# Performance work log

Hardware: AMD Instinct MI355X
Metric: run time of the kernel (lower is better)

## Reference

```python
import jax, jax.numpy as jnp
import numpy as np

DIM = 1024
H = 16
D = DIM // H  # head_dim = 64
SCALE = D ** (-0.5)


def _gate_mlp(x, w1, b1, w2, b2):
    # Linear -> ReLU -> Linear -> Sigmoid
    h = jax.nn.relu(x @ w1 + b1)
    return jax.nn.sigmoid(h @ w2 + b2)


def _heads(t, B, N):
    # [B,N,C] -> [B,H,N,D]
    return t.reshape(B, N, H, D).transpose(0, 2, 1, 3)


def setup_inputs() -> dict:
    key = jax.random.key(0)
    ks = jax.random.split(key, 12)
    s = 1.0 / np.sqrt(DIM)
    inp = {
        "x1": jax.random.normal(ks[0], (4, 4096, DIM), jnp.float32),
        "x2": jax.random.normal(ks[1], (4, 4096, DIM), jnp.float32),
        # kv projections (no bias, qkv_bias=False); stored as [in, out]
        "Wkv1": jax.random.normal(ks[2], (DIM, 2 * DIM), jnp.float32) * s,
        "Wkv2": jax.random.normal(ks[3], (DIM, 2 * DIM), jnp.float32) * s,
        # gate MLP 1
        "g1_w1": jax.random.normal(ks[4], (DIM, DIM), jnp.float32) * s,
        "g1_b1": jnp.zeros((DIM,), jnp.float32),
        "g1_w2": jax.random.normal(ks[5], (DIM, DIM), jnp.float32) * s,
        "g1_b2": jnp.zeros((DIM,), jnp.float32),
        # gate MLP 2
        "g2_w1": jax.random.normal(ks[6], (DIM, DIM), jnp.float32) * s,
        "g2_b1": jnp.zeros((DIM,), jnp.float32),
        "g2_w2": jax.random.normal(ks[7], (DIM, DIM), jnp.float32) * s,
        "g2_b2": jnp.zeros((DIM,), jnp.float32),
    }
    return inp


def reference(x1, x2, Wkv1, Wkv2, g1_w1, g1_b1, g1_w2, g1_b2, g2_w1, g2_b1, g2_w2, g2_b2):
    B, N, C = x1.shape

    q1 = _heads(x1, B, N)  # [B,H,N,D]
    q2 = _heads(x2, B, N)

    kv1 = (x1 @ Wkv1).reshape(B, N, 2, H, D).transpose(2, 0, 3, 1, 4)
    k1, v1 = kv1[0], kv1[1]  # [B,H,N,D]
    kv2 = (x2 @ Wkv2).reshape(B, N, 2, H, D).transpose(2, 0, 3, 1, 4)
    k2, v2 = kv2[0], kv2[1]

    gate1 = _heads(_gate_mlp(x1, g1_w1, g1_b1, g1_w2, g1_b2), B, N)
    gate2 = _heads(_gate_mlp(x2, g2_w1, g2_b1, g2_w2, g2_b2), B, N)

    # context: k^T @ (v*gate) -> [B,H,D,D], softmax over first D axis (dim=-2)
    ctx1 = jnp.einsum('bhnd,bhne->bhde', k1, v1 * gate1) * SCALE
    ctx1 = jax.nn.softmax(ctx1, axis=-2)
    ctx2 = jnp.einsum('bhnd,bhne->bhde', k2, v2 * gate2) * SCALE
    ctx2 = jax.nn.softmax(ctx2, axis=-2)

    # cross: x1 attends via ctx2, x2 via ctx1
    o1 = jnp.einsum('bhnd,bhde->bhne', q1, ctx2).transpose(0, 2, 1, 3).reshape(B, N, C)
    o2 = jnp.einsum('bhnd,bhde->bhne', q2, ctx1).transpose(0, 2, 1, 3).reshape(B, N, C)
    return (o1, o2)
```

## Files before the change

### kernel.cpp

```cpp
#include <hip/hip_runtime.h>
#include <hip/hip_bf16.h>

typedef __attribute__((ext_vector_type(8))) short bf16x8_t;
typedef __attribute__((ext_vector_type(4))) float f32x4_t;
typedef unsigned short u16;
typedef unsigned int u32;

#define GLL16(gp, lp) \
    __builtin_amdgcn_global_load_lds((const __attribute__((address_space(1))) u32*)(gp), \
                                     (__attribute__((address_space(3))) u32*)(lp), 16, 0, 0)

__device__ __forceinline__ float bf2f(unsigned int u16v) {
    union { unsigned int i; float f; } c;
    c.i = (u16v & 0xffffu) << 16;
    return c.f;
}
__device__ __forceinline__ unsigned short f2bf(float f) {
    union { float f; unsigned int i; } c; c.f = f;
    unsigned int x = c.i;
    unsigned int r = (x + 0x7fffu + ((x >> 16) & 1u)) >> 16;
    return (unsigned short)r;
}


__global__ void cast_x2_kernel(const float* __restrict__ x1, const float* __restrict__ x2,
                               u16* __restrict__ h1, u16* __restrict__ h2, int n4) {
    int i = blockIdx.x * blockDim.x + threadIdx.x;
    int stride = gridDim.x * blockDim.x;
    for (; i < n4; i += stride) {
        float4 v = *(const float4*)(x1 + (size_t)i * 4);
        ushort4 h;
        h.x = f2bf(v.x); h.y = f2bf(v.y); h.z = f2bf(v.z); h.w = f2bf(v.w);
        *(ushort4*)(h1 + (size_t)i * 4) = h;
        v = *(const float4*)(x2 + (size_t)i * 4);
        h.x = f2bf(v.x); h.y = f2bf(v.y); h.z = f2bf(v.z); h.w = f2bf(v.w);
        *(ushort4*)(h2 + (size_t)i * 4) = h;
    }
}

__global__ __launch_bounds__(256) void cast_wt4_kernel(
    const float* __restrict__ W0, const float* __restrict__ W1,
    const float* __restrict__ W2, const float* __restrict__ W3,
    u16* __restrict__ T0, u16* __restrict__ T1,
    u16* __restrict__ T2, u16* __restrict__ T3,
    int K, int N) {
    const float* W = (blockIdx.z == 0) ? W0 : (blockIdx.z == 1) ? W1 : (blockIdx.z == 2) ? W2 : W3;
    u16* Wt = (blockIdx.z == 0) ? T0 : (blockIdx.z == 1) ? T1 : (blockIdx.z == 2) ? T2 : T3;
    __shared__ u16 tile[32][33];
    int c0 = blockIdx.x * 32, k0 = blockIdx.y * 32;
    int tx = threadIdx.x & 31, ty = threadIdx.x >> 5;
#pragma unroll
    for (int i = 0; i < 4; ++i) {
        int k = k0 + ty + i * 8;
        tile[ty + i * 8][tx] = f2bf(W[(size_t)k * N + c0 + tx]);
    }
    __syncthreads();
#pragma unroll
    for (int i = 0; i < 4; ++i) {
        int c = c0 + ty + i * 8;
        Wt[(size_t)c * K + k0 + tx] = tile[tx][ty + i * 8];
    }
}

__global__ __launch_bounds__(256) void cast_wt_split2_kernel(
    const float* __restrict__ W0, const float* __restrict__ W1,
    u16* __restrict__ H0, u16* __restrict__ L0,
    u16* __restrict__ H1, u16* __restrict__ L1,
    int K, int N) {
    const float* W = blockIdx.z ? W1 : W0;
    u16* Wh = blockIdx.z ? H1 : H0;
    u16* Wl = blockIdx.z ? L1 : L0;
    __shared__ u16 th[32][33];
    __shared__ u16 tl[32][33];
    int c0 = blockIdx.x * 32, k0 = blockIdx.y * 32;
    int tx = threadIdx.x & 31, ty = threadIdx.x >> 5;
#pragma unroll
    for (int i = 0; i < 4; ++i) {
        int k = k0 + ty + i * 8;
        float f = W[(size_t)k * N + c0 + tx];
        unsigned short h = f2bf(f);
        th[ty + i * 8][tx] = h;
        tl[ty + i * 8][tx] = f2bf(f - bf2f(h));
    }
    __syncthreads();
#pragma unroll
    for (int i = 0; i < 4; ++i) {
        int c = c0 + ty + i * 8;
        Wh[(size_t)c * K + k0 + tx] = th[tx][ty + i * 8];
        Wl[(size_t)c * K + k0 + tx] = tl[tx][ty + i * 8];
    }
}


__device__ __forceinline__ void stage32(u16* lds_buf, const u16* __restrict__ gbase, int tid) {
#pragma unroll
    for (int g = 0; g < 2; ++g) {
        int c = tid + g * 256;
        int row = c >> 2, qp = c & 3;
        int qs = qp ^ ((row >> 1) & 3);
        GLL16(gbase + (size_t)row * 1024 + qs * 8, lds_buf + c * 8);
    }
}

template <int EPI>
__global__ __launch_bounds__(256, 4) void gemm128_kernel(
    const u16* __restrict__ Ah,
    const u16* __restrict__ Bh, const u16* __restrict__ Bl,
    const float* __restrict__ bias,
    u16* __restrict__ out_bf, float* __restrict__ out_f,
    float* __restrict__ gate_vg, float* __restrict__ kout,
    int N)
{
    __shared__ u16 As[2][4096];
    __shared__ u16 Bs[2][4096];
    const int NT = (EPI == 2) ? 64 : 32;

    int nwg = 128 * (N >> 7);
    int wg = blockIdx.y * 128 + blockIdx.x;
    int cpx = nwg >> 3;
    wg = (wg & 7) * cpx + (wg >> 3);
    int bx = wg & 127, by = wg >> 7;
    int row0 = bx << 7, col0 = by << 7;

    const int tid = threadIdx.x;
    const int lane = tid & 63;
    const int w = tid >> 6;
    const int wm = w >> 1, wn = w & 1;
    const int fr = lane & 15, fq = lane >> 4;

    const u16* Ab0 = Ah + (size_t)row0 * 1024;
    auto aslice = [&](int s) { return Ab0 + s * 32; };
    auto bbase = [&](int kt) -> const u16* {
        if (EPI == 2) return ((kt & 1) ? Bl : Bh) + (size_t)col0 * 1024 + (kt >> 1) * 32;
        return Bh + (size_t)col0 * 1024 + kt * 32;
    };

    f32x4_t acc[4][4];
#pragma unroll
    for (int m = 0; m < 4; ++m)
#pragma unroll
        for (int n = 0; n < 4; ++n) acc[m][n] = (f32x4_t)(0.0f);

    const int slot = (fq ^ ((fr >> 1) & 3)) * 8;
    int aoff[4], boff[4];
#pragma unroll
    for (int m = 0; m < 4; ++m) aoff[m] = (wm * 64 + m * 16 + fr) * 32 + slot;
#pragma unroll
    for (int n = 0; n < 4; ++n) boff[n] = (wn * 64 + n * 16 + fr) * 32 + slot;

    stage32(As[0], aslice(0), tid);
    stage32(Bs[0], bbase(0), tid);

    for (int kt = 0; kt < NT; ++kt) {
        __syncthreads();

        if (kt + 1 < NT) {
            stage32(Bs[(kt + 1) & 1], bbase(kt + 1), tid);
            if (EPI == 2) {
                int s1 = (kt >> 1) + 1;
                if ((kt & 1) == 0 && s1 < 32)
                    stage32(As[s1 & 1], aslice(s1), tid);
            } else {
                stage32(As[(kt + 1) & 1], aslice(kt + 1), tid);
            }
        }

        const int ab = (EPI == 2) ? ((kt >> 1) & 1) : (kt & 1);
        const int bb = kt & 1;
        bf16x8_t a[4], b[4];
#pragma unroll
        for (int m = 0; m < 4; ++m) a[m] = *(const bf16x8_t*)&As[ab][aoff[m]];
#pragma unroll
        for (int n = 0; n < 4; ++n) b[n] = *(const bf16x8_t*)&Bs[bb][boff[n]];
#pragma unroll
        for (int m = 0; m < 4; ++m)
#pragma unroll
            for (int n = 0; n < 4; ++n)
                acc[m][n] = __builtin_amdgcn_mfma_f32_16x16x32_bf16(a[m], b[n], acc[m][n], 0, 0, 0);
    }

#pragma unroll
    for (int m = 0; m < 4; ++m) {
        int row = row0 + wm * 64 + m * 16 + fq * 4;
#pragma unroll
        for (int n = 0; n < 4; ++n) {
            int col = col0 + wn * 64 + n * 16 + fr;
            if (EPI == 0) {
                float bv = bias[col];
#pragma unroll
                for (int rr = 0; rr < 4; ++rr)
                    out_bf[(size_t)(row + rr) * N + col] = f2bf(fmaxf(acc[m][n][rr] + bv, 0.0f));
            } else if (EPI == 1) {
                float bv = bias[col];
#pragma unroll
                for (int rr = 0; rr < 4; ++rr)
                    out_f[(size_t)(row + rr) * N + col] = 1.0f / (1.0f + __expf(-(acc[m][n][rr] + bv)));
            } else {
                if (col < 1024) {
#pragma unroll
                    for (int rr = 0; rr < 4; ++rr)
                        kout[(size_t)(row + rr) * 1024 + col] = acc[m][n][rr];
                } else {
#pragma unroll
                    for (int rr = 0; rr < 4; ++rr) {
                        size_t idx = (size_t)(row + rr) * 1024 + (col - 1024);
                        gate_vg[idx] = acc[m][n][rr] * gate_vg[idx];
                    }
                }
            }
        }
    }
}

__global__ __launch_bounds__(256) void ctx_part_kernel(
    const float* __restrict__ kmat,
    const float* __restrict__ vmat,
    float* __restrict__ part)
{
    int bh = blockIdx.x & 63;
    int p  = blockIdx.x >> 6;
    int b = bh >> 4, h = bh & 15;
    int n0 = p * 512;
    __shared__ float ks[128][64];
    __shared__ float vs[128][64];
    int t = threadIdx.x;
    int dg = t & 15, eg = t >> 4;
    float acc[4][4];
#pragma unroll
    for (int i = 0; i < 4; ++i)
#pragma unroll
        for (int j = 0; j < 4; ++j) acc[i][j] = 0.0f;

    const float* kb = kmat + (size_t)b * 4096 * 1024 + h * 64;
    const float* vb = vmat + (size_t)b * 4096 * 1024 + h * 64;

    for (int c0 = 0; c0 < 512; c0 += 128) {
        __syncthreads();
#pragma unroll
        for (int s = 0; s < 8; ++s) {
            int ci = t + s * 256;
            int r = ci >> 4, o4 = (ci & 15) * 4;
            size_t g = (size_t)(n0 + c0 + r) * 1024 + o4;
            *(float4*)(&ks[r][o4]) = *(const float4*)(kb + g);
            *(float4*)(&vs[r][o4]) = *(const float4*)(vb + g);
        }
        __syncthreads();
#pragma unroll 4
        for (int n = 0; n < 128; ++n) {
            float4 k4 = *(const float4*)(&ks[n][dg * 4]);
            float4 v4 = *(const float4*)(&vs[n][eg * 4]);
            acc[0][0] += k4.x * v4.x; acc[0][1] += k4.x * v4.y; acc[0][2] += k4.x * v4.z; acc[0][3] += k4.x * v4.w;
            acc[1][0] += k4.y * v4.x; acc[1][1] += k4.y * v4.y; acc[1][2] += k4.y * v4.z; acc[1][3] += k4.y * v4.w;
            acc[2][0] += k4.z * v4.x; acc[2][1] += k4.z * v4.y; acc[2][2] += k4.z * v4.z; acc[2][3] += k4.z * v4.w;
            acc[3][0] += k4.w * v4.x; acc[3][1] += k4.w * v4.y; acc[3][2] += k4.w * v4.z; acc[3][3] += k4.w * v4.w;
        }
    }
    float* pp = part + ((size_t)(p * 64 + bh)) * 64 * 64;
#pragma unroll
    for (int i = 0; i < 4; ++i)
#pragma unroll
        for (int j = 0; j < 4; ++j)
            pp[(dg * 4 + i) * 64 + (eg * 4 + j)] = acc[i][j];
}

__global__ __launch_bounds__(256) void softmax_ctx_kernel(const float* __restrict__ part,
                                                          float* __restrict__ ctx) {
    int bh = blockIdx.x;
    int t = threadIdx.x;
    int e = t & 63, dq = t >> 6;
    __shared__ float red[4][68];
    float loc[16];
    float m = -1e30f;
#pragma unroll
    for (int i = 0; i < 16; ++i) {
        int d = dq * 16 + i;
        float s = 0.f;
#pragma unroll
        for (int p = 0; p < 8; ++p)
            s += part[(((size_t)(p * 64 + bh)) * 64 + d) * 64 + e];
        s *= 0.125f;
        loc[i] = s;
        m = fmaxf(m, s);
    }
    red[dq][e] = m;
    __syncthreads();
    float M = fmaxf(fmaxf(red[0][e], red[1][e]), fmaxf(red[2][e], red[3][e]));
    float sum = 0.f;
#pragma unroll
    for (int i = 0; i < 16; ++i) {
        float v = __expf(loc[i] - M);
        loc[i] = v;
        sum += v;
    }
    __syncthreads();
    red[dq][e] = sum;
    __syncthreads();
    float inv = 1.0f / (red[0][e] + red[1][e] + red[2][e] + red[3][e]);
#pragma unroll
    for (int i = 0; i < 16; ++i) {
        int d = dq * 16 + i;
        ctx[((size_t)bh * 64 + d) * 64 + e] = loc[i] * inv;
    }
}

__global__ __launch_bounds__(256) void out_gemm_kernel(
    const float* __restrict__ x1, const float* __restrict__ x2,
    const float* __restrict__ ctxA,
    const float* __restrict__ ctxB,
    float* __restrict__ out)
{
    int id = blockIdx.x;
    int s = id >> 12;
    int r = id & 4095;
    int nc = r & 63;
    int h = (r >> 6) & 15;
    int b = r >> 10;
    const float* x = s ? x2 : x1;
    const float* ctx = s ? ctxB : ctxA;
    float* o = out + (size_t)s * 16777216;
    size_t r0 = (size_t)b * 4096 + nc * 64;
    __shared__ float xs[64][65];
    __shared__ float cs[64][64];
    int t = threadIdx.x;
    for (int idx = t; idx < 4096; idx += 256) {
        int rr = idx >> 6, d = idx & 63;
        xs[rr][d] = x[(r0 + rr) * 1024 + h * 64 + d];
    }
    const float* cb = ctx + ((size_t)(b * 16 + h)) * 4096;
    for (int idx = t; idx < 4096; idx += 256) {
        cs[idx >> 6][idx & 63] = cb[idx];
    }
    __syncthreads();
    int eg = t & 15, nl = t >> 4;
    for (int rr = nl; rr < 64; rr += 16) {
        float a0 = 0.f, a1 = 0.f, a2 = 0.f, a3 = 0.f;
#pragma unroll
        for (int d = 0; d < 64; ++d) {
            float xv = xs[rr][d];
            float4 cv = *(const float4*)(&cs[d][eg * 4]);
            a0 += xv * cv.x; a1 += xv * cv.y; a2 += xv * cv.z; a3 += xv * cv.w;
        }
        float4 ov = make_float4(a0, a1, a2, a3);
        *(float4*)(&o[(r0 + rr) * 1024 + h * 64 + eg * 4]) = ov;
    }
}


extern "C" void kernel_launch(void* const* d_in, const int* in_sizes, int n_in,
                              void* d_out, int out_size, void* d_ws, size_t ws_size,
                              hipStream_t stream)
{
    (void)in_sizes; (void)n_in; (void)out_size; (void)ws_size;
    const float* x1   = (const float*)d_in[0];
    const float* x2   = (const float*)d_in[1];
    const float* Wkv1 = (const float*)d_in[2];
    const float* Wkv2 = (const float*)d_in[3];
    const float* g1w1 = (const float*)d_in[4];
    const float* g1b1 = (const float*)d_in[5];
    const float* g1w2 = (const float*)d_in[6];
    const float* g1b2 = (const float*)d_in[7];
    const float* g2w1 = (const float*)d_in[8];
    const float* g2b1 = (const float*)d_in[9];
    const float* g2w2 = (const float*)d_in[10];
    const float* g2b2 = (const float*)d_in[11];
    float* out = (float*)d_out;

    char* ws = (char*)d_ws;
    size_t off = 0;
    auto alloc = [&](size_t b) { void* p = ws + off; off += (b + 255) & ~(size_t)255; return p; };
    const size_t NTOK = 16384;
    u16* xh1   = (u16*)alloc(NTOK * 1024 * 2);
    u16* xh2   = (u16*)alloc(NTOK * 1024 * 2);
    u16* wkv1h = (u16*)alloc((size_t)2048 * 1024 * 2);
    u16* wkv1l = (u16*)alloc((size_t)2048 * 1024 * 2);
    u16* wkv2h = (u16*)alloc((size_t)2048 * 1024 * 2);
    u16* wkv2l = (u16*)alloc((size_t)2048 * 1024 * 2);
    u16* g1w1t = (u16*)alloc((size_t)1024 * 1024 * 2);
    u16* g1w2t = (u16*)alloc((size_t)1024 * 1024 * 2);
    u16* g2w1t = (u16*)alloc((size_t)1024 * 1024 * 2);
    u16* g2w2t = (u16*)alloc((size_t)1024 * 1024 * 2);
    u16* hbuf  = (u16*)alloc(NTOK * 1024 * 2);
    float* gate = (float*)alloc(NTOK * 1024 * 4);
    float* kbuf = (float*)alloc(NTOK * 1024 * 4);
    float* part = (float*)alloc((size_t)8 * 64 * 64 * 64 * 4);
    float* ctx1 = (float*)alloc((size_t)64 * 64 * 64 * 4);
    float* ctx2 = (float*)alloc((size_t)64 * 64 * 64 * 4);

    cast_wt_split2_kernel<<<dim3(64, 32, 2), 256, 0, stream>>>(Wkv1, Wkv2,
                                                               wkv1h, wkv1l, wkv2h, wkv2l, 1024, 2048);
    cast_wt4_kernel<<<dim3(32, 32, 4), 256, 0, stream>>>(g1w1, g1w2, g2w1, g2w2,
                                                         g1w1t, g1w2t, g2w1t, g2w2t, 1024, 1024);
    cast_x2_kernel<<<2048, 256, 0, stream>>>(x1, x2, xh1, xh2, (int)(NTOK * 1024 / 4));

    gemm128_kernel<0><<<dim3(128, 8), 256, 0, stream>>>(xh1, g1w1t, nullptr, g1b1,
                                                        hbuf, nullptr, nullptr, nullptr, 1024);
    gemm128_kernel<1><<<dim3(128, 8), 256, 0, stream>>>(hbuf, g1w2t, nullptr, g1b2,
                                                        nullptr, gate, nullptr, nullptr, 1024);
    gemm128_kernel<2><<<dim3(128, 16), 256, 0, stream>>>(xh1, wkv1h, wkv1l, nullptr,
                                                         nullptr, nullptr, gate, kbuf, 2048);
    ctx_part_kernel<<<512, 256, 0, stream>>>(kbuf, gate, part);
    softmax_ctx_kernel<<<64, 256, 0, stream>>>(part, ctx1);

    gemm128_kernel<0><<<dim3(128, 8), 256, 0, stream>>>(xh2, g2w1t, nullptr, g2b1,
                                                        hbuf, nullptr, nullptr, nullptr, 1024);
    gemm128_kernel<1><<<dim3(128, 8), 256, 0, stream>>>(hbuf, g2w2t, nullptr, g2b2,
                                                        nullptr, gate, nullptr, nullptr, 1024);
    gemm128_kernel<2><<<dim3(128, 16), 256, 0, stream>>>(xh2, wkv2h, wkv2l, nullptr,
                                                         nullptr, nullptr, gate, kbuf, 2048);
    ctx_part_kernel<<<512, 256, 0, stream>>>(kbuf, gate, part);
    softmax_ctx_kernel<<<64, 256, 0, stream>>>(part, ctx2);

    out_gemm_kernel<<<8192, 256, 0, stream>>>(x1, x2, ctx2, ctx1, out);
}
```

Baseline: 932.0 us.

## Use bf16 MFMA for output projection with transposed bf16 context

Replaces the fp32 scalar shared-memory output GEMM (q @ ctx) with an MFMA bf16 kernel that reads the already-cast bf16 inputs and a transposed bf16 context written by the softmax kernel. Each wave computes a 64x64 tile directly from global memory with no shared memory staging. This cuts ALU work and the fp32 input reads, at the cost of bf16 rounding of q and the softmax context, plus uncoalesced scalar output stores.

```diff
diff --git a/kernel.cpp b/kernel.cpp
--- a/kernel.cpp
+++ b/kernel.cpp
@@ -264,7 +264,7 @@
 }
 
 __global__ __launch_bounds__(256) void softmax_ctx_kernel(const float* __restrict__ part,
-                                                          float* __restrict__ ctx) {
+                                                          u16* __restrict__ ctxT) {
     int bh = blockIdx.x;
     int t = threadIdx.x;
     int e = t & 63, dq = t >> 6;
@@ -296,52 +296,67 @@
     red[dq][e] = sum;
     __syncthreads();
     float inv = 1.0f / (red[0][e] + red[1][e] + red[2][e] + red[3][e]);
-#pragma unroll
-    for (int i = 0; i < 16; ++i) {
-        int d = dq * 16 + i;
-        ctx[((size_t)bh * 64 + d) * 64 + e] = loc[i] * inv;
-    }
-}
-
-__global__ __launch_bounds__(256) void out_gemm_kernel(
-    const float* __restrict__ x1, const float* __restrict__ x2,
-    const float* __restrict__ ctxA,
-    const float* __restrict__ ctxB,
+    u16* op = ctxT + ((size_t)bh * 64 + e) * 64 + dq * 16;
+#pragma unroll
+    for (int i = 0; i < 16; ++i)
+        op[i] = f2bf(loc[i] * inv);
+}
+
+__global__ __launch_bounds__(256) void out_mfma_kernel(
+    const u16* __restrict__ xh1, const u16* __restrict__ xh2,
+    const u16* __restrict__ ctxTA,
+    const u16* __restrict__ ctxTB,
     float* __restrict__ out)
 {
     int id = blockIdx.x;
-    int s = id >> 12;
-    int r = id & 4095;
-    int nc = r & 63;
-    int h = (r >> 6) & 15;
-    int b = r >> 10;
-    const float* x = s ? x2 : x1;
-    const float* ctx = s ? ctxB : ctxA;
+    int s = id >> 10;
+    int r = id & 1023;
+    int b = r >> 8;
+    int h = (r >> 4) & 15;
+    int rc = r & 15;
+    const u16* xh = s ? xh2 : xh1;
+    const u16* ctxT = s ? ctxTB : ctxTA;
     float* o = out + (size_t)s * 16777216;
-    size_t r0 = (size_t)b * 4096 + nc * 64;
-    __shared__ float xs[64][65];
-    __shared__ float cs[64][64];
-    int t = threadIdx.x;
-    for (int idx = t; idx < 4096; idx += 256) {
-        int rr = idx >> 6, d = idx & 63;
-        xs[rr][d] = x[(r0 + rr) * 1024 + h * 64 + d];
-    }
-    const float* cb = ctx + ((size_t)(b * 16 + h)) * 4096;
-    for (int idx = t; idx < 4096; idx += 256) {
-        cs[idx >> 6][idx & 63] = cb[idx];
-    }
-    __syncthreads();
-    int eg = t & 15, nl = t >> 4;
-    for (int rr = nl; rr < 64; rr += 16) {
-        float a0 = 0.f, a1 = 0.f, a2 = 0.f, a3 = 0.f;
-#pragma unroll
-        for (int d = 0; d < 64; ++d) {
-            float xv = xs[rr][d];
-            float4 cv = *(const float4*)(&cs[d][eg * 4]);
-            a0 += xv * cv.x; a1 += xv * cv.y; a2 += xv * cv.z; a3 += xv * cv.w;
+
+    int tid = threadIdx.x, lane = tid & 63, w = tid >> 6;
+    int fr = lane & 15, fq = lane >> 4;
+    size_t rowbase = (size_t)b * 4096 + rc * 256 + w * 64;
+    const u16* Ab = xh + rowbase * 1024 + h * 64;
+    const u16* Bb = ctxT + ((size_t)(b * 16 + h)) * 4096;
+
+    f32x4_t acc[4][4];
+#pragma unroll
+    for (int m = 0; m < 4; ++m)
+#pragma unroll
+        for (int n = 0; n < 4; ++n) acc[m][n] = (f32x4_t)(0.0f);
+
+#pragma unroll
+    for (int ks = 0; ks < 2; ++ks) {
+        bf16x8_t a[4], bfr[4];
+#pragma unroll
+        for (int m = 0; m < 4; ++m)
+            a[m] = *(const bf16x8_t*)(Ab + (size_t)(m * 16 + fr) * 1024 + ks * 32 + fq * 8);
+#pragma unroll
+        for (int n = 0; n < 4; ++n)
+            bfr[n] = *(const bf16x8_t*)(Bb + (n * 16 + fr) * 64 + ks * 32 + fq * 8);
+#pragma unroll
+        for (int m = 0; m < 4; ++m)
+#pragma unroll
+            for (int n = 0; n < 4; ++n)
+                acc[m][n] = __builtin_amdgcn_mfma_f32_16x16x32_bf16(a[m], bfr[n], acc[m][n], 0, 0, 0);
+    }
+
+#pragma unroll
+    for (int m = 0; m < 4; ++m) {
+#pragma unroll
+        for (int n = 0; n < 4; ++n) {
+            int col = h * 64 + n * 16 + fr;
+#pragma unroll
+            for (int rr = 0; rr < 4; ++rr) {
+                size_t row = rowbase + m * 16 + fq * 4 + rr;
+                o[row * 1024 + col] = acc[m][n][rr];
+            }
         }
-        float4 ov = make_float4(a0, a1, a2, a3);
-        *(float4*)(&o[(r0 + rr) * 1024 + h * 64 + eg * 4]) = ov;
     }
 }
 
@@ -383,8 +398,8 @@
     float* gate = (float*)alloc(NTOK * 1024 * 4);
     float* kbuf = (float*)alloc(NTOK * 1024 * 4);
     float* part = (float*)alloc((size_t)8 * 64 * 64 * 64 * 4);
-    float* ctx1 = (float*)alloc((size_t)64 * 64 * 64 * 4);
-    float* ctx2 = (float*)alloc((size_t)64 * 64 * 64 * 4);
+    u16* ctxT1 = (u16*)alloc((size_t)64 * 64 * 64 * 2);
+    u16* ctxT2 = (u16*)alloc((size_t)64 * 64 * 64 * 2);
 
     cast_wt_split2_kernel<<<dim3(64, 32, 2), 256, 0, stream>>>(Wkv1, Wkv2,
                                                                wkv1h, wkv1l, wkv2h, wkv2l, 1024, 2048);
@@ -399,7 +414,7 @@
     gemm128_kernel<2><<<dim3(128, 16), 256, 0, stream>>>(xh1, wkv1h, wkv1l, nullptr,
                                                          nullptr, nullptr, gate, kbuf, 2048);
     ctx_part_kernel<<<512, 256, 0, stream>>>(kbuf, gate, part);
-    softmax_ctx_kernel<<<64, 256, 0, stream>>>(part, ctx1);
+    softmax_ctx_kernel<<<64, 256, 0, stream>>>(part, ctxT1);
 
     gemm128_kernel<0><<<dim3(128, 8), 256, 0, stream>>>(xh2, g2w1t, nullptr, g2b1,
                                                         hbuf, nullptr, nullptr, nullptr, 1024);
@@ -408,7 +423,7 @@
     gemm128_kernel<2><<<dim3(128, 16), 256, 0, stream>>>(xh2, wkv2h, wkv2l, nullptr,
                                                          nullptr, nullptr, gate, kbuf, 2048);
     ctx_part_kernel<<<512, 256, 0, stream>>>(kbuf, gate, part);
-    softmax_ctx_kernel<<<64, 256, 0, stream>>>(part, ctx2);
-
-    out_gemm_kernel<<<8192, 256, 0, stream>>>(x1, x2, ctx2, ctx1, out);
-}
+    softmax_ctx_kernel<<<64, 256, 0, stream>>>(part, ctxT2);
+
+    out_mfma_kernel<<<2048, 256, 0, stream>>>(xh1, xh2, ctxT2, ctxT1, out);
+}
```

Result: faster. 758.0 us (-18.7%).
